# Kernel optimization log

Measured on AMD Instinct MI355X. Metric: run time of the kernel, lower is better.

Reference implementation:

```python
import jax, jax.numpy as jnp
import numpy as np

B, S, D = 2, 2048, 1024
H = 16
HD = D // H

def setup_inputs() -> dict:
    key = jax.random.key(0)
    ks = jax.random.split(key, 9)
    scale = 1.0 / np.sqrt(D)
    return {
        "qi": jax.random.normal(ks[0], (B, S, D), jnp.float32),
        "ki": jax.random.normal(ks[1], (B, S, D), jnp.float32),
        "vi": jax.random.normal(ks[2], (B, S, D), jnp.float32),
        "Wq": jax.random.normal(ks[3], (D, D), jnp.float32) * scale,
        "Wq_def": jax.random.normal(ks[4], (D, D), jnp.float32) * scale,
        "Wk": jax.random.normal(ks[5], (D, D), jnp.float32) * scale,
        "Wk_def": jax.random.normal(ks[6], (D, D), jnp.float32) * scale,
        "Wv": jax.random.normal(ks[7], (D, D), jnp.float32) * scale,
        "Wo": jax.random.normal(ks[8], (D, D), jnp.float32) * scale,
    }

def _heads(x, W):
    # torch Linear: x @ W.T, then view (B,S,H,HD) and transpose -> (B,H,S,HD)
    return (x @ W.T).reshape(B, S, H, HD).transpose(0, 2, 1, 3)

def reference(qi, ki, vi, Wq, Wq_def, Wk, Wk_def, Wv, Wo):
    q = _heads(qi, Wq)
    q_def = _heads(qi, Wq_def)
    k = _heads(ki, Wk)
    k_def = _heads(ki, Wk_def)
    v = _heads(vi, Wv)
    inv_sqrt = 1.0 / jnp.sqrt(jnp.asarray(HD, qi.dtype))
    scores = jnp.einsum('bhse,bhte->bhst', q, k) * inv_sqrt
    def_scores = jnp.einsum('bhse,bhte->bhst', q_def, k_def) * inv_sqrt
    # defeasible weights: sigmoid(def_scores).sum over t -> [B,H,S], broadcast over query dim
    def_w = jax.nn.sigmoid(def_scores).sum(axis=3)  # [B,H,S]
    attn = jax.nn.softmax(scores * def_w[:, :, None, :], axis=-1)
    attended = jnp.einsum('bhst,bhtd->bshd', attn, v).reshape(B, S, D)
    return attended @ Wo.T
```

## Files before the change

kernel.cpp:

```cpp
#include <hip/hip_runtime.h>
#include <math.h>

#define BSZ 2
#define SEQ 2048
#define DIM 1024
#define NH 16
#define HDIM 64
#define MR (BSZ*SEQ)

typedef __attribute__((ext_vector_type(8))) short bf16x8;
typedef __attribute__((ext_vector_type(4))) short bf16x4;
typedef __attribute__((ext_vector_type(4))) float floatx4;
typedef _Float16 f16x8 __attribute__((ext_vector_type(8)));

static __device__ __forceinline__ unsigned short f2bf(float x) {
    unsigned u = __float_as_uint(x);
    u += 0x7fffu + ((u >> 16) & 1u);
    return (unsigned short)(u >> 16);
}
static __device__ __forceinline__ float bf2f(unsigned short h) {
    return __uint_as_float(((unsigned)h) << 16);
}
static __device__ __forceinline__ unsigned short f2h(float x) {
    union { _Float16 h; unsigned short u; } v;
    v.h = (_Float16)x;
    return v.u;
}
static __device__ __forceinline__ float fexp2(float x) {
#if __has_builtin(__builtin_amdgcn_exp2f)
    return __builtin_amdgcn_exp2f(x);
#else
    return __expf(x * 0.69314718055994531f);
#endif
}
static __device__ __forceinline__ bf16x4 pack_bf16x4(float a, float b, float c, float d) {
    union { unsigned u[2]; bf16x4 v; } r;
    asm("v_cvt_pk_bf16_f32 %0, %1, %2" : "=v"(r.u[0]) : "v"(a), "v"(b));
    asm("v_cvt_pk_bf16_f32 %0, %1, %2" : "=v"(r.u[1]) : "v"(c), "v"(d));
    return r.v;
}
#define MFMA16(a,b,c) __builtin_amdgcn_mfma_f32_16x16x32_bf16((a),(b),(c),0,0,0)

static __device__ __forceinline__ floatx4 mfma_f16(bf16x8 a, bf16x8 b, floatx4 c) {
    union { bf16x8 s; f16x8 h; } ua, ub;
    ua.s = a; ub.s = b;
    return __builtin_amdgcn_mfma_f32_16x16x32_f16(ua.h, ub.h, c, 0, 0, 0);
}

static __device__ __forceinline__ floatx4 pv_mfma(bf16x4 a, bf16x4 b, floatx4 c) {
#if __has_builtin(__builtin_amdgcn_mfma_f32_16x16x16bf16_1k)
    return __builtin_amdgcn_mfma_f32_16x16x16bf16_1k(a, b, c, 0, 0, 0);
#else
    bf16x8 a8 = {a[0],a[1],a[2],a[3],0,0,0,0};
    bf16x8 b8 = {b[0],b[1],b[2],b[3],0,0,0,0};
    return MFMA16(a8, b8, c);
#endif
}

static __device__ __forceinline__ void gld16(const void* g, void* l) {
    __builtin_amdgcn_global_load_lds(
        (const __attribute__((address_space(1))) void*)g,
        (__attribute__((address_space(3))) void*)l, 16, 0, 0);
}

__global__ __launch_bounds__(256)
void conv_split(const float* p0, const float* p1, const float* p2,
                const float* p3,
                unsigned short* o0, unsigned short* o1, unsigned short* o2,
                unsigned short* o3,
                int r0, int r1, int r2, int r3)
{
    const float* pin; unsigned short* pout; int rows;
    switch (blockIdx.y) {
        case 0: pin=p0; pout=o0; rows=r0; break;
        case 1: pin=p1; pout=o1; rows=r1; break;
        case 2: pin=p2; pout=o2; rows=r2; break;
        default: pin=p3; pout=o3; rows=r3; break;
    }
    size_t idx = (size_t)blockIdx.x * 256 + threadIdx.x;
    if (idx * 4 >= (size_t)rows * DIM) return;
    size_t row = (idx * 4) >> 10;
    int col = (int)((idx * 4) & 1023);
    float4 f = *(const float4*)(pin + idx * 4);
    ushort4 h, l;
    h.x = f2bf(f.x); l.x = f2bf(f.x - bf2f(h.x));
    h.y = f2bf(f.y); l.y = f2bf(f.y - bf2f(h.y));
    h.z = f2bf(f.z); l.z = f2bf(f.z - bf2f(h.z));
    h.w = f2bf(f.w); l.w = f2bf(f.w - bf2f(h.w));
    *(ushort4*)(pout + row * 2048 + col)        = h;
    *(ushort4*)(pout + row * 2048 + 1024 + col) = l;
}

__global__ __launch_bounds__(256)
void conv_f16(const float* p0, const float* p1, const float* p2, const float* p3,
              unsigned short* o0, unsigned short* o1, unsigned short* o2,
              unsigned short* o3, int r0, int r1, int r2, int r3)
{
    const float* pin; unsigned short* pout; int rows;
    switch (blockIdx.y) {
        case 0: pin=p0; pout=o0; rows=r0; break;
        case 1: pin=p1; pout=o1; rows=r1; break;
        case 2: pin=p2; pout=o2; rows=r2; break;
        default: pin=p3; pout=o3; rows=r3; break;
    }
    size_t idx = (size_t)blockIdx.x * 256 + threadIdx.x;
    if (idx * 4 >= (size_t)rows * DIM) return;
    float4 f = *(const float4*)(pin + idx * 4);
    ushort4 h;
    h.x = f2h(f.x); h.y = f2h(f.y); h.z = f2h(f.z); h.w = f2h(f.w);
    *(ushort4*)(pout + idx * 4) = h;
}

__global__ __launch_bounds__(256)
void conv_hi(const float* p0, const float* p1, const float* p2,
             unsigned short* o0, unsigned short* o1, unsigned short* o2,
             int n0, int n1, int n2)
{
    const float* pin; unsigned short* pout; int n;
    switch (blockIdx.y) {
        case 0: pin=p0; pout=o0; n=n0; break;
        case 1: pin=p1; pout=o1; n=n1; break;
        default: pin=p2; pout=o2; n=n2; break;
    }
    size_t idx = (size_t)blockIdx.x * 256 + threadIdx.x;
    if (idx * 4 >= (size_t)n) return;
    float4 f = *(const float4*)(pin + idx * 4);
    ushort4 h;
    h.x = f2bf(f.x); h.y = f2bf(f.y); h.z = f2bf(f.z); h.w = f2bf(f.w);
    *(ushort4*)(pout + idx * 4) = h;
}

template<int EPI, bool SPLIT3, int DT>
__global__ __launch_bounds__(256)
void gemm_mfma(const unsigned short* __restrict__ A0, const unsigned short* __restrict__ A1,
               const unsigned short* __restrict__ B0, const unsigned short* __restrict__ B1,
               void* C0v, void* C1v, int lda, int ldb, int nkb)
{
    const unsigned short* A = blockIdx.z ? A1 : A0;
    const unsigned short* B = blockIdx.z ? B1 : B0;
    float* Cf = (float*)(blockIdx.z ? C1v : C0v);
    unsigned short* Cb = (unsigned short*)(blockIdx.z ? C1v : C0v);

    __shared__ __align__(16) unsigned short As[128][72];
    __shared__ __align__(16) unsigned short Bs[128][72];

    const int tid = threadIdx.x;
    const int lane = tid & 63, wv = tid >> 6;
    const int c = lane & 15, quad = lane >> 4;
    const int wm = wv >> 1, wn = wv & 1;
    const int rowBase = blockIdx.y << 7;
    const int colBase = blockIdx.x << 7;

    floatx4 acc[4][4];
#pragma unroll
    for (int i = 0; i < 4; ++i)
#pragma unroll
        for (int j = 0; j < 4; ++j) acc[i][j] = (floatx4){0.f,0.f,0.f,0.f};

    bf16x8 ar[4], br[4];
    {
#pragma unroll
        for (int i = 0; i < 4; ++i) {
            int f = tid + (i << 8);
            int r = f >> 3, kbk = (f & 7) << 3;
            ar[i] = *(const bf16x8*)(A + (size_t)(rowBase + r) * lda + kbk);
            br[i] = *(const bf16x8*)(B + (size_t)(colBase + r) * ldb + kbk);
        }
    }
    for (int kb = 0; kb < nkb; ++kb) {
        __syncthreads();
#pragma unroll
        for (int i = 0; i < 4; ++i) {
            int f = tid + (i << 8);
            int r = f >> 3, kbk = (f & 7) << 3;
            *(bf16x8*)&As[r][kbk] = ar[i];
            *(bf16x8*)&Bs[r][kbk] = br[i];
        }
        __syncthreads();
        if (kb + 1 < nkb) {
            int kn = kb + 1, aoff, boff;
            if (SPLIT3) {
                int t = kn >> 4, kk = (kn & 15) << 6;
                aoff = ((t == 1) ? 1024 : 0) + kk;
                boff = ((t == 2) ? 1024 : 0) + kk;
            } else { aoff = boff = kn << 6; }
#pragma unroll
            for (int i = 0; i < 4; ++i) {
                int f = tid + (i << 8);
                int r = f >> 3, kbk = (f & 7) << 3;
                ar[i] = *(const bf16x8*)(A + (size_t)(rowBase + r) * lda + aoff + kbk);
                br[i] = *(const bf16x8*)(B + (size_t)(colBase + r) * ldb + boff + kbk);
            }
        }
#pragma unroll
        for (int ks = 0; ks < 2; ++ks) {
            bf16x8 af[4], bfr[4];
#pragma unroll
            for (int i = 0; i < 4; ++i) {
                af[i]  = *(const bf16x8*)&As[wm*64 + i*16 + c][ks*32 + quad*8];
                bfr[i] = *(const bf16x8*)&Bs[wn*64 + i*16 + c][ks*32 + quad*8];
            }
#pragma unroll
            for (int mi = 0; mi < 4; ++mi)
#pragma unroll
                for (int ni = 0; ni < 4; ++ni) {
                    if (DT == 0) acc[mi][ni] = MFMA16(af[mi], bfr[ni], acc[mi][ni]);
                    else         acc[mi][ni] = mfma_f16(af[mi], bfr[ni], acc[mi][ni]);
                }
        }
    }
    const int row0 = rowBase + wm*64 + quad*4;
    if (EPI == 0) {
        const int col0 = colBase + wn*64 + c;
#pragma unroll
        for (int mi = 0; mi < 4; ++mi)
#pragma unroll
            for (int r = 0; r < 4; ++r) {
                size_t ro = (size_t)(row0 + mi*16 + r) * 1024 + col0;
#pragma unroll
                for (int ni = 0; ni < 4; ++ni)
                    Cf[ro + ni*16] = acc[mi][ni][r];
            }
    } else if (EPI == 1) {
        const int h = (colBase >> 6) + wn;
#pragma unroll
        for (int mi = 0; mi < 4; ++mi)
#pragma unroll
            for (int r = 0; r < 4; ++r) {
                int row = row0 + mi*16 + r;
                int b = row >> 11, s = row & 2047;
                size_t base = ((size_t)((b<<4) | h) * 2048 + s) * 128;
                const int sw = (s & 7) << 3;
#pragma unroll
                for (int ni = 0; ni < 4; ++ni) {
                    int d = ni*16 + c;
                    int dsw = d ^ sw;
                    float x = acc[mi][ni][r];
                    unsigned short hb = f2bf(x);
                    Cb[base + dsw]      = hb;
                    Cb[base + 64 + dsw] = f2bf(x - bf2f(hb));
                }
            }
    } else if (EPI == 2) {
        const int h = (colBase >> 6) + wn;
#pragma unroll
        for (int mi = 0; mi < 4; ++mi) {
            int row = row0 + mi*16;
            int b = row >> 11, s = row & 2047;
#pragma unroll
            for (int ni = 0; ni < 4; ++ni) {
                int d = ni*16 + c;
                int scol = s ^ ((d & 7) << 3);
                size_t base = ((size_t)((b<<4)|h) * 64 + d) * 2048 + scol;
                ushort4 o4;
                o4.x = f2bf(acc[mi][ni][0]); o4.y = f2bf(acc[mi][ni][1]);
                o4.z = f2bf(acc[mi][ni][2]); o4.w = f2bf(acc[mi][ni][3]);
                *(ushort4*)(Cb + base) = o4;
            }
        }
    } else {
        const int h = (colBase >> 6) + wn;
#pragma unroll
        for (int mi = 0; mi < 4; ++mi)
#pragma unroll
            for (int r = 0; r < 4; ++r) {
                int row = row0 + mi*16 + r;
                int b = row >> 11, s = row & 2047;
                size_t base = ((size_t)((b<<4) | h) * 2048 + s) * 64;
#pragma unroll
                for (int ni = 0; ni < 4; ++ni)
                    Cb[base + ni*16 + c] = f2h(acc[mi][ni][r]);
            }
    }
}

__global__ __launch_bounds__(256)
void defw_mfma(const unsigned short* __restrict__ qd,
               const unsigned short* __restrict__ kd,
               float* __restrict__ defw)
{
    __shared__ __align__(16) unsigned short Ks[64][72];
    const int tid = threadIdx.x;
    const int wv = tid >> 6, lane = tid & 63;
    const int c = lane & 15, quad = lane >> 4;
    const int bh = blockIdx.y;
    const int qbase = blockIdx.x << 7;
    const int trow = tid >> 2, seg = tid & 3;

    bf16x8 qf[2][2];
#pragma unroll
    for (int mi = 0; mi < 2; ++mi) {
        const unsigned short* qrow =
            qd + ((size_t)bh*2048 + qbase + wv*32 + mi*16 + c)*64 + quad*8;
        qf[mi][0] = *(const bf16x8*)(qrow);
        qf[mi][1] = *(const bf16x8*)(qrow + 32);
    }
    float rs[2][4] = {{0.f,0.f,0.f,0.f},{0.f,0.f,0.f,0.f}};
    const unsigned short* kbase = kd + (size_t)bh*2048*64;
    bf16x8 kpre[2];
    {
        const unsigned short* kp = kbase + (size_t)trow*64 + seg*16;
        kpre[0] = *(const bf16x8*)(kp);
        kpre[1] = *(const bf16x8*)(kp + 8);
    }
    for (int kt = 0; kt < SEQ; kt += 64) {
        __syncthreads();
        *(bf16x8*)&Ks[trow][seg*16 + 0] = kpre[0];
        *(bf16x8*)&Ks[trow][seg*16 + 8] = kpre[1];
        __syncthreads();
        if (kt + 64 < SEQ) {
            const unsigned short* kp = kbase + (size_t)(kt + 64 + trow)*64 + seg*16;
            kpre[0] = *(const bf16x8*)(kp);
            kpre[1] = *(const bf16x8*)(kp + 8);
        }
#pragma unroll
        for (int nk = 0; nk < 4; ++nk) {
            const unsigned short* kr = &Ks[16*nk + c][quad*8];
            bf16x8 k0 = *(const bf16x8*)(kr);
            bf16x8 k1 = *(const bf16x8*)(kr + 32);
#pragma unroll
            for (int mi = 0; mi < 2; ++mi) {
                floatx4 s = {0.f,0.f,0.f,0.f};
                s = mfma_f16(qf[mi][0], k0, s);
                s = mfma_f16(qf[mi][1], k1, s);
#pragma unroll
                for (int r = 0; r < 4; ++r)
                    rs[mi][r] += 1.f / (1.f + __expf(-0.125f * s[r]));
            }
        }
    }
#pragma unroll
    for (int mi = 0; mi < 2; ++mi)
#pragma unroll
        for (int r = 0; r < 4; ++r) {
            float vv = rs[mi][r];
            vv += __shfl_xor(vv, 1, 16);
            vv += __shfl_xor(vv, 2, 16);
            vv += __shfl_xor(vv, 4, 16);
            vv += __shfl_xor(vv, 8, 16);
            if (c == 0)
                defw[(size_t)bh*SEQ + qbase + wv*32 + mi*16 + 4*quad + r]
                    = vv * 0.18033688011112042f;
        }
}

__global__ __launch_bounds__(512)
void flash_mfma(const unsigned short* __restrict__ q,
                const unsigned short* __restrict__ kk,
                const unsigned short* __restrict__ vt,
                const float* __restrict__ dwg,
                unsigned short* __restrict__ o)
{
    __shared__ __align__(16) unsigned short Ks[2][64][128];
    __shared__ __align__(16) unsigned short Vs[2][64][64];
    __shared__ __align__(16) float dwL[SEQ];
    const int tid = threadIdx.x;
    const int wv = tid >> 6, lane = tid & 63;
    const int c = lane & 15, quad = lane >> 4;
    const int cswz = c & 7;
    const int bh = blockIdx.y, b = bh >> 4, h = bh & 15;
    const int qbase = blockIdx.x << 7;

    const unsigned short* kbase = kk + (size_t)bh*2048*128;
    const unsigned short* vbase = vt + (size_t)bh*64*2048;

    bf16x8 qhi[2], qlo[2];
    {
        const unsigned short* qrow =
            q + ((size_t)bh*2048 + qbase + wv*16 + c)*128;
        qhi[0] = *(const bf16x8*)(qrow + (((quad     ) ^ cswz) << 3));
        qhi[1] = *(const bf16x8*)(qrow + (((quad +  4) ^ cswz) << 3));
        qlo[0] = *(const bf16x8*)(qrow + (((quad +  8) ^ cswz) << 3));
        qlo[1] = *(const bf16x8*)(qrow + (((quad + 12) ^ cswz) << 3));
    }
    gld16(dwg + (size_t)bh*SEQ + (size_t)tid*4, &dwL[(wv*64) * 4]);
#pragma unroll
    for (int i = 0; i < 2; ++i) {
        int flat = tid + (i << 9);
        int r = flat >> 4, ch = flat & 15;
        gld16(kbase + (size_t)r*128 + (ch << 3),
              &Ks[0][0][0] + ((wv*64 + (i << 9)) << 3));
    }
    {
        int d = tid >> 3, ch = tid & 7;
        gld16(vbase + (size_t)d*2048 + (ch << 3),
              &Vs[0][0][0] + (wv*64 << 3));
    }

    floatx4 Oa[4];
#pragma unroll
    for (int nd = 0; nd < 4; ++nd) Oa[nd] = (floatx4){0.f,0.f,0.f,0.f};
    float mrun = -3.0e38f, lrun = 0.f;

#define FLASH_TILE(CUR, KT, PF)                                               \
    {                                                                         \
        __builtin_amdgcn_s_barrier();                                         \
        if (PF) {                                                             \
            _Pragma("unroll")                                                 \
            for (int i = 0; i < 2; ++i) {                                     \
                int flat = tid + (i << 9);                                    \
                int r = flat >> 4, ch = flat & 15;                            \
                gld16(kbase + (size_t)((KT) + 64 + r)*128 + (ch << 3),        \
                      &Ks[(CUR)^1][0][0] + ((wv*64 + (i << 9)) << 3));        \
            }                                                                 \
            {                                                                 \
                int d = tid >> 3, ch = tid & 7;                               \
                gld16(vbase + (size_t)d*2048 + ((KT) + 64) + (ch << 3),       \
                      &Vs[(CUR)^1][0][0] + (wv*64 << 3));                     \
            }                                                                 \
            asm volatile("s_waitcnt vmcnt(3)" ::: "memory");                  \
        } else {                                                              \
            asm volatile("s_waitcnt vmcnt(0)" ::: "memory");                  \
        }                                                                     \
        __builtin_amdgcn_s_barrier();                                         \
        __builtin_amdgcn_sched_barrier(0);                                    \
        float z[4][4];                                                        \
        _Pragma("unroll")                                                     \
        for (int nk = 0; nk < 4; ++nk) {                                      \
            const unsigned short* krow = &Ks[CUR][16*nk + c][0];              \
            bf16x8 kh0 = *(const bf16x8*)(krow + (((quad     ) ^ cswz) << 3));\
            bf16x8 kh1 = *(const bf16x8*)(krow + (((quad +  4) ^ cswz) << 3));\
            bf16x8 kl0 = *(const bf16x8*)(krow + (((quad +  8) ^ cswz) << 3));\
            bf16x8 kl1 = *(const bf16x8*)(krow + (((quad + 12) ^ cswz) << 3));\
            float4 d4 = *(const float4*)&dwL[(KT) + nk*16 + quad*4];          \
            floatx4 s = {0.f,0.f,0.f,0.f};                                    \
            __builtin_amdgcn_s_setprio(1);                                    \
            s = MFMA16(kh0, qhi[0], s);                                       \
            s = MFMA16(kh1, qhi[1], s);                                       \
            s = MFMA16(kh0, qlo[0], s);                                       \
            s = MFMA16(kh1, qlo[1], s);                                       \
            s = MFMA16(kl0, qhi[0], s);                                       \
            s = MFMA16(kl1, qhi[1], s);                                       \
            __builtin_amdgcn_s_setprio(0);                                    \
            z[nk][0] = s[0] * d4.x;                                           \
            z[nk][1] = s[1] * d4.y;                                           \
            z[nk][2] = s[2] * d4.z;                                           \
            z[nk][3] = s[3] * d4.w;                                           \
        }                                                                     \
        {                                                                     \
            float tm = z[0][0];                                               \
            _Pragma("unroll")                                                 \
            for (int nk = 0; nk < 4; ++nk)                                    \
                _Pragma("unroll")                                             \
                for (int r = 0; r < 4; ++r) tm = fmaxf(tm, z[nk][r]);         \
            tm = fmaxf(tm, __shfl_xor(tm, 16));                               \
            tm = fmaxf(tm, __shfl_xor(tm, 32));                               \
            if (__any(tm > mrun)) {                                           \
                float mn = fmaxf(mrun, tm);                                   \
                float al = fexp2(mrun - mn);                                  \
                mrun = mn;                                                    \
                lrun *= al;                                                   \
                _Pragma("unroll")                                             \
                for (int nd = 0; nd < 4; ++nd)                                \
                    _Pragma("unroll")                                         \
                    for (int r = 0; r < 4; ++r)                               \
                        Oa[nd][r] *= al;                                      \
            }                                                                 \
            float rsum = 0.f;                                                 \
            _Pragma("unroll")                                                 \
            for (int nk = 0; nk < 4; ++nk)                                    \
                _Pragma("unroll")                                             \
                for (int r = 0; r < 4; ++r) {                                 \
                    z[nk][r] = fexp2(z[nk][r] - mrun);                        \
                    rsum += z[nk][r];                                         \
                }                                                             \
            rsum += __shfl_xor(rsum, 16);                                     \
            rsum += __shfl_xor(rsum, 32);                                     \
            lrun += rsum;                                                     \
        }                                                                     \
        bf16x4 pb[4];                                                         \
        _Pragma("unroll")                                                     \
        for (int nk = 0; nk < 4; ++nk)                                        \
            pb[nk] = pack_bf16x4(z[nk][0], z[nk][1], z[nk][2], z[nk][3]);     \
        __builtin_amdgcn_s_setprio(1);                                        \
        _Pragma("unroll")                                                     \
        for (int ks = 0; ks < 4; ++ks) {                                      \
            const int vch = ((2*ks + (quad >> 1)) ^ cswz);                    \
            _Pragma("unroll")                                                 \
            for (int nd = 0; nd < 4; ++nd) {                                  \
                const bf16x4 va = *(const bf16x4*)                            \
                    (&Vs[CUR][nd*16 + c][0] + (vch << 3) + ((quad & 1) << 2));\
                Oa[nd] = pv_mfma(va, pb[ks], Oa[nd]);                         \
            }                                                                 \
        }                                                                     \
        __builtin_amdgcn_s_setprio(0);                                        \
    }

    for (int kt = 0; kt < SEQ; kt += 128) {
        FLASH_TILE(0, kt, 1)
        FLASH_TILE(1, kt + 64, kt + 128 < SEQ)
    }
#undef FLASH_TILE

    {
        float invl = 1.f / lrun;
        int s_abs = qbase + wv*16 + c;
        unsigned short* orow = o + ((size_t)(b*SEQ + s_abs))*DIM + h*HDIM;
#pragma unroll
        for (int nd = 0; nd < 4; ++nd) {
            ushort4 o4;
            o4.x = f2bf(Oa[nd][0] * invl);
            o4.y = f2bf(Oa[nd][1] * invl);
            o4.z = f2bf(Oa[nd][2] * invl);
            o4.w = f2bf(Oa[nd][3] * invl);
            *(ushort4*)(orow + nd*16 + quad*4) = o4;
        }
    }
}

extern "C" void kernel_launch(void* const* d_in, const int* in_sizes, int n_in,
                              void* d_out, int out_size, void* d_ws, size_t ws_size,
                              hipStream_t stream)
{
    (void)in_sizes; (void)n_in; (void)out_size; (void)ws_size;
    const float* qi     = (const float*)d_in[0];
    const float* ki     = (const float*)d_in[1];
    const float* vi     = (const float*)d_in[2];
    const float* Wq     = (const float*)d_in[3];
    const float* Wq_def = (const float*)d_in[4];
    const float* Wk     = (const float*)d_in[5];
    const float* Wk_def = (const float*)d_in[6];
    const float* Wv     = (const float*)d_in[7];
    const float* Wo     = (const float*)d_in[8];
    float* out = (float*)d_out;

    char* ws = (char*)d_ws;
    const size_t MB = 1024 * 1024;
    unsigned short* Aqf  = (unsigned short*)(ws +  0*MB);
    unsigned short* Akf  = (unsigned short*)(ws +  8*MB);
    unsigned short* Bqdf = (unsigned short*)(ws + 16*MB);
    unsigned short* Bkdf = (unsigned short*)(ws + 18*MB);
    unsigned short* qdf  = (unsigned short*)(ws + 20*MB);
    unsigned short* kdf  = (unsigned short*)(ws + 28*MB);
    unsigned short* Aq  = (unsigned short*)(ws +  0*MB);
    unsigned short* Ak  = (unsigned short*)(ws + 16*MB);
    unsigned short* Bq  = (unsigned short*)(ws + 32*MB);
    unsigned short* Bk  = (unsigned short*)(ws + 36*MB);
    unsigned short* qs  = (unsigned short*)(ws + 40*MB);
    unsigned short* ks  = (unsigned short*)(ws + 56*MB);
    float*          dw  = (float*)(ws + 72*MB);
    unsigned short* Av  = (unsigned short*)(ws +  0*MB);
    unsigned short* Bv  = (unsigned short*)(ws +  8*MB);
    unsigned short* Bo  = (unsigned short*)(ws + 10*MB);
    unsigned short* Vt  = (unsigned short*)(ws + 12*MB);
    unsigned short* att = (unsigned short*)(ws + 20*MB);

    dim3 cb(256);
    dim3 gP(DIM/128, MR/128, 2);
    dim3 gS(DIM/128, MR/128, 1);
    dim3 gA(SEQ/128, BSZ*NH);

    conv_f16<<<dim3(4096, 4), cb, 0, stream>>>(
        qi, ki, Wq_def, Wk_def, Aqf, Akf, Bqdf, Bkdf, MR, MR, DIM, DIM);
    gemm_mfma<3, false, 1><<<gP, cb, 0, stream>>>(Aqf, Akf, Bqdf, Bkdf, qdf, kdf, 1024, 1024, 16);
    defw_mfma<<<gA, cb, 0, stream>>>(qdf, kdf, dw);
    conv_split<<<dim3(4096, 4), cb, 0, stream>>>(
        qi, ki, Wq, Wk, Aq, Ak, Bq, Bk, MR, MR, DIM, DIM);
    gemm_mfma<1, true, 0><<<gP, cb, 0, stream>>>(Aq, Ak, Bq, Bk, qs, ks, 2048, 2048, 48);
    conv_hi<<<dim3(4096, 3), cb, 0, stream>>>(vi, Wv, Wo, Av, Bv, Bo,
                                              MR*DIM, DIM*DIM, DIM*DIM);
    gemm_mfma<2, false, 0><<<gS, cb, 0, stream>>>(Av, Av, Bv, Bv, Vt, Vt, 1024, 1024, 16);
    flash_mfma<<<gA, dim3(512), 0, stream>>>(qs, ks, Vt, dw, att);
    gemm_mfma<0, false, 0><<<gS, cb, 0, stream>>>(att, att, Bo, Bo, out, out, 1024, 1024, 16);
}
```

Before: 428.1 us.

## Use direct global-to-LDS loads in GEMM and widen defw blocks to 512 threads

The GEMM main loop drops its register prefetch pipeline and fills unpadded shared tiles with gld16 direct global-to-LDS loads, issued fresh each k-step between barriers. This saves registers and LDS-write instructions, but removes the overlap of the next tile's loads with MFMA compute and may add LDS bank conflicts because the rows are no longer padded. Separately, defw_mfma now runs 512 threads per block, each wave handling 16 query rows instead of 32. That roughly halves per-thread work and raises parallelism, at the cost of more redundant K-tile loads per output row.

```diff
diff --git a/kernel.cpp b/kernel.cpp
--- a/kernel.cpp
+++ b/kernel.cpp
@@ -141,8 +141,8 @@
     float* Cf = (float*)(blockIdx.z ? C1v : C0v);
     unsigned short* Cb = (unsigned short*)(blockIdx.z ? C1v : C0v);
 
-    __shared__ __align__(16) unsigned short As[128][72];
-    __shared__ __align__(16) unsigned short Bs[128][72];
+    __shared__ __align__(16) unsigned short As[128][64];
+    __shared__ __align__(16) unsigned short Bs[128][64];
 
     const int tid = threadIdx.x;
     const int lane = tid & 63, wv = tid >> 6;
@@ -157,41 +157,24 @@
 #pragma unroll
         for (int j = 0; j < 4; ++j) acc[i][j] = (floatx4){0.f,0.f,0.f,0.f};
 
-    bf16x8 ar[4], br[4];
-    {
+    for (int kb = 0; kb < nkb; ++kb) {
+        int aoff, boff;
+        if (SPLIT3) {
+            int t = kb >> 4, kk = (kb & 15) << 6;
+            aoff = ((t == 1) ? 1024 : 0) + kk;
+            boff = ((t == 2) ? 1024 : 0) + kk;
+        } else { aoff = boff = kb << 6; }
+        __syncthreads();
 #pragma unroll
         for (int i = 0; i < 4; ++i) {
             int f = tid + (i << 8);
-            int r = f >> 3, kbk = (f & 7) << 3;
-            ar[i] = *(const bf16x8*)(A + (size_t)(rowBase + r) * lda + kbk);
-            br[i] = *(const bf16x8*)(B + (size_t)(colBase + r) * ldb + kbk);
-        }
-    }
-    for (int kb = 0; kb < nkb; ++kb) {
-        __syncthreads();
-#pragma unroll
-        for (int i = 0; i < 4; ++i) {
-            int f = tid + (i << 8);
-            int r = f >> 3, kbk = (f & 7) << 3;
-            *(bf16x8*)&As[r][kbk] = ar[i];
-            *(bf16x8*)&Bs[r][kbk] = br[i];
+            int r = f >> 3, ch = (f & 7) << 3;
+            gld16(A + (size_t)(rowBase + r) * lda + aoff + ch,
+                  &As[0][0] + (size_t)f * 8);
+            gld16(B + (size_t)(colBase + r) * ldb + boff + ch,
+                  &Bs[0][0] + (size_t)f * 8);
         }
         __syncthreads();
-        if (kb + 1 < nkb) {
-            int kn = kb + 1, aoff, boff;
-            if (SPLIT3) {
-                int t = kn >> 4, kk = (kn & 15) << 6;
-                aoff = ((t == 1) ? 1024 : 0) + kk;
-                boff = ((t == 2) ? 1024 : 0) + kk;
-            } else { aoff = boff = kn << 6; }
-#pragma unroll
-            for (int i = 0; i < 4; ++i) {
-                int f = tid + (i << 8);
-                int r = f >> 3, kbk = (f & 7) << 3;
-                ar[i] = *(const bf16x8*)(A + (size_t)(rowBase + r) * lda + aoff + kbk);
-                br[i] = *(const bf16x8*)(B + (size_t)(colBase + r) * ldb + boff + kbk);
-            }
-        }
 #pragma unroll
         for (int ks = 0; ks < 2; ++ks) {
             bf16x8 af[4], bfr[4];
@@ -274,7 +257,7 @@
     }
 }
 
-__global__ __launch_bounds__(256)
+__global__ __launch_bounds__(512)
 void defw_mfma(const unsigned short* __restrict__ qd,
                const unsigned short* __restrict__ kd,
                float* __restrict__ defw)
@@ -285,63 +268,48 @@
     const int c = lane & 15, quad = lane >> 4;
     const int bh = blockIdx.y;
     const int qbase = blockIdx.x << 7;
-    const int trow = tid >> 2, seg = tid & 3;
-
-    bf16x8 qf[2][2];
-#pragma unroll
-    for (int mi = 0; mi < 2; ++mi) {
+    const int trow = tid >> 3, seg = tid & 7;
+
+    bf16x8 qf[2];
+    {
         const unsigned short* qrow =
-            qd + ((size_t)bh*2048 + qbase + wv*32 + mi*16 + c)*64 + quad*8;
-        qf[mi][0] = *(const bf16x8*)(qrow);
-        qf[mi][1] = *(const bf16x8*)(qrow + 32);
-    }
-    float rs[2][4] = {{0.f,0.f,0.f,0.f},{0.f,0.f,0.f,0.f}};
+            qd + ((size_t)bh*2048 + qbase + wv*16 + c)*64 + quad*8;
+        qf[0] = *(const bf16x8*)(qrow);
+        qf[1] = *(const bf16x8*)(qrow + 32);
+    }
+    float rs[4] = {0.f,0.f,0.f,0.f};
     const unsigned short* kbase = kd + (size_t)bh*2048*64;
-    bf16x8 kpre[2];
-    {
-        const unsigned short* kp = kbase + (size_t)trow*64 + seg*16;
-        kpre[0] = *(const bf16x8*)(kp);
-        kpre[1] = *(const bf16x8*)(kp + 8);
-    }
+    bf16x8 kpre = *(const bf16x8*)(kbase + (size_t)trow*64 + seg*8);
     for (int kt = 0; kt < SEQ; kt += 64) {
         __syncthreads();
-        *(bf16x8*)&Ks[trow][seg*16 + 0] = kpre[0];
-        *(bf16x8*)&Ks[trow][seg*16 + 8] = kpre[1];
+        *(bf16x8*)&Ks[trow][seg*8] = kpre;
         __syncthreads();
-        if (kt + 64 < SEQ) {
-            const unsigned short* kp = kbase + (size_t)(kt + 64 + trow)*64 + seg*16;
-            kpre[0] = *(const bf16x8*)(kp);
-            kpre[1] = *(const bf16x8*)(kp + 8);
-        }
+        if (kt + 64 < SEQ)
+            kpre = *(const bf16x8*)(kbase + (size_t)(kt + 64 + trow)*64 + seg*8);
 #pragma unroll
         for (int nk = 0; nk < 4; ++nk) {
             const unsigned short* kr = &Ks[16*nk + c][quad*8];
             bf16x8 k0 = *(const bf16x8*)(kr);
             bf16x8 k1 = *(const bf16x8*)(kr + 32);
-#pragma unroll
-            for (int mi = 0; mi < 2; ++mi) {
-                floatx4 s = {0.f,0.f,0.f,0.f};
-                s = mfma_f16(qf[mi][0], k0, s);
-                s = mfma_f16(qf[mi][1], k1, s);
-#pragma unroll
-                for (int r = 0; r < 4; ++r)
-                    rs[mi][r] += 1.f / (1.f + __expf(-0.125f * s[r]));
-            }
+            floatx4 s = {0.f,0.f,0.f,0.f};
+            s = mfma_f16(qf[0], k0, s);
+            s = mfma_f16(qf[1], k1, s);
+#pragma unroll
+            for (int r = 0; r < 4; ++r)
+                rs[r] += 1.f / (1.f + __expf(-0.125f * s[r]));
         }
     }
 #pragma unroll
-    for (int mi = 0; mi < 2; ++mi)
-#pragma unroll
-        for (int r = 0; r < 4; ++r) {
-            float vv = rs[mi][r];
-            vv += __shfl_xor(vv, 1, 16);
-            vv += __shfl_xor(vv, 2, 16);
-            vv += __shfl_xor(vv, 4, 16);
-            vv += __shfl_xor(vv, 8, 16);
-            if (c == 0)
-                defw[(size_t)bh*SEQ + qbase + wv*32 + mi*16 + 4*quad + r]
-                    = vv * 0.18033688011112042f;
-        }
+    for (int r = 0; r < 4; ++r) {
+        float vv = rs[r];
+        vv += __shfl_xor(vv, 1, 16);
+        vv += __shfl_xor(vv, 2, 16);
+        vv += __shfl_xor(vv, 4, 16);
+        vv += __shfl_xor(vv, 8, 16);
+        if (c == 0)
+            defw[(size_t)bh*SEQ + qbase + wv*16 + 4*quad + r]
+                = vv * 0.18033688011112042f;
+    }
 }
 
 __global__ __launch_bounds__(512)
@@ -553,7 +521,7 @@
     conv_f16<<<dim3(4096, 4), cb, 0, stream>>>(
         qi, ki, Wq_def, Wk_def, Aqf, Akf, Bqdf, Bkdf, MR, MR, DIM, DIM);
     gemm_mfma<3, false, 1><<<gP, cb, 0, stream>>>(Aqf, Akf, Bqdf, Bkdf, qdf, kdf, 1024, 1024, 16);
-    defw_mfma<<<gA, cb, 0, stream>>>(qdf, kdf, dw);
+    defw_mfma<<<gA, dim3(512), 0, stream>>>(qdf, kdf, dw);
     conv_split<<<dim3(4096, 4), cb, 0, stream>>>(
         qi, ki, Wq, Wk, Aq, Ak, Bq, Bk, MR, MR, DIM, DIM);
     gemm_mfma<1, true, 0><<<gP, cb, 0, stream>>>(Aq, Ak, Bq, Bk, qs, ks, 2048, 2048, 48);
```

Measured after the change: 444.6 us. 1.04x slower.
